# Kernel optimization log

Hardware: AMD Instinct MI355X
Metric: run time of the kernel (lower is better)

Reference implementation:

```python
import jax, jax.numpy as jnp
import numpy as np

B, L, D = 2, 1024, 768
NH, HD = 12, 64
NL = 6
MLP = 3072
THETA = 10000.0


def _rope(pos, dim, theta):
    # pos: (L,) float -> (L, dim//2, 2, 2) rotation matrices (FLUX rope)
    omega = 1.0 / (theta ** (jnp.arange(0, dim, 2, dtype=jnp.float32) / dim))
    out = pos[:, None] * omega  # (L, dim//2)
    cos, sin = jnp.cos(out), jnp.sin(out)
    return jnp.stack([jnp.stack([cos, -sin], -1), jnp.stack([sin, cos], -1)], -2)


def _build_pe(seq_len, pe_dim):
    # 2D spatial ids: axis0 = x (fast), axis1 = y (slow); axes_dim = [pe_dim//2, pe_dim//2]
    h = w = int(seq_len ** 0.5)
    y_ids = jnp.repeat(jnp.arange(h, dtype=jnp.float32), w)
    x_ids = jnp.tile(jnp.arange(w, dtype=jnp.float32), h)
    half = pe_dim // 2
    pe = jnp.concatenate([_rope(x_ids, half, THETA), _rope(y_ids, half, THETA)], axis=-3)
    return pe[None, None]  # (1, 1, L, pe_dim//2, 2, 2)


def _apply_rope(x, pe):
    # x: (B, H, L, HD)
    xs = x.reshape(x.shape[:-1] + (-1, 1, 2))
    out = pe[..., 0] * xs[..., 0] + pe[..., 1] * xs[..., 1]
    return out.reshape(x.shape)


def _rmsnorm(x, scale):
    return x * jax.lax.rsqrt(jnp.mean(x * x, axis=-1, keepdims=True) + 1e-6) * scale


def _layernorm(x, g, b):
    m = jnp.mean(x, axis=-1, keepdims=True)
    v = jnp.var(x, axis=-1, keepdims=True)
    return (x - m) * jax.lax.rsqrt(v + 1e-5) * g + b


def _forward(spatial_features, density_weights, condition_embeddings,
             spatial_w, spatial_b, cond_w, cond_b,
             ln1_g, ln1_b, qkv_w, q_scale, k_scale, proj_w, proj_b,
             dscale, dbias, ln2_g, ln2_b, mlp_w1, mlp_b1, mlp_w2, mlp_b2,
             out_w, out_b):
    Bsz, Ls, Ds = spatial_features.shape
    x = spatial_features @ spatial_w + spatial_b
    x = x + (condition_embeddings @ cond_w + cond_b)[:, None, :]
    pe = _build_pe(Ls, HD)
    dflat = density_weights.reshape(Bsz, 1, Ls)  # H*W == L, no interpolation
    attn_scale = HD ** -0.5
    for i in range(NL):
        h = _layernorm(x, ln1_g[i], ln1_b[i])
        qkv = (h @ qkv_w[i]).reshape(Bsz, Ls, 3, NH, HD).transpose(2, 0, 3, 1, 4)
        q, k, v = qkv[0], qkv[1], qkv[2]
        q = _rmsnorm(q, q_scale[i])
        k = _rmsnorm(k, k_scale[i])
        q = _apply_rope(q, pe)
        k = _apply_rope(k, pe)
        scores = jnp.einsum('bhld,bhmd->bhlm', q, k) * attn_scale
        scores = scores + (dscale[i] * dflat[..., None] + dbias[i])  # (B,1,L,1) bcast
        attn = jax.nn.softmax(scores, axis=-1)
        o = jnp.einsum('bhlm,bhmd->bhld', attn, v)
        o = o.transpose(0, 2, 1, 3).reshape(Bsz, Ls, Ds)
        x = x + o @ proj_w[i] + proj_b[i]
        h2 = _layernorm(x, ln2_g[i], ln2_b[i])
        x = x + jax.nn.gelu(h2 @ mlp_w1[i] + mlp_b1[i], approximate=False) @ mlp_w2[i] + mlp_b2[i]
    return x @ out_w + out_b


def setup_inputs() -> dict:
    key = jax.random.key(0)
    ks = jax.random.split(key, 16)
    s = 0.02
    inp = {
        'spatial_features': jax.random.normal(ks[0], (B, L, D), jnp.float32),
        'density_weights': jax.random.uniform(ks[1], (B, 32, 32), jnp.float32),
        'condition_embeddings': jax.random.normal(ks[2], (B, 1536), jnp.float32),
        'spatial_w': jax.random.normal(ks[3], (D, D), jnp.float32) * s,
        'spatial_b': jnp.zeros((D,), jnp.float32),
        'cond_w': jax.random.normal(ks[4], (1536, D), jnp.float32) * s,
        'cond_b': jnp.zeros((D,), jnp.float32),
        'ln1_g': jnp.ones((NL, D), jnp.float32),
        'ln1_b': jnp.zeros((NL, D), jnp.float32),
        'qkv_w': jax.random.normal(ks[5], (NL, D, 3 * D), jnp.float32) * s,
        'q_scale': jnp.ones((NL, HD), jnp.float32),
        'k_scale': jnp.ones((NL, HD), jnp.float32),
        'proj_w': jax.random.normal(ks[6], (NL, D, D), jnp.float32) * s,
        'proj_b': jnp.zeros((NL, D), jnp.float32),
        'dscale': jnp.ones((NL,), jnp.float32),
        'dbias': jnp.zeros((NL,), jnp.float32),
        'ln2_g': jnp.ones((NL, D), jnp.float32),
        'ln2_b': jnp.zeros((NL, D), jnp.float32),
        'mlp_w1': jax.random.normal(ks[7], (NL, D, MLP), jnp.float32) * s,
        'mlp_b1': jnp.zeros((NL, MLP), jnp.float32),
        'mlp_w2': jax.random.normal(ks[8], (NL, MLP, D), jnp.float32) * s,
        'mlp_b2': jnp.zeros((NL, D), jnp.float32),
        'out_w': jax.random.normal(ks[9], (D, D), jnp.float32) * s,
        'out_b': jnp.zeros((D,), jnp.float32),
    }
    return inp


def reference(spatial_features, density_weights, condition_embeddings,
              spatial_w, spatial_b, cond_w, cond_b,
              ln1_g, ln1_b, qkv_w, q_scale, k_scale, proj_w, proj_b,
              dscale, dbias, ln2_g, ln2_b, mlp_w1, mlp_b1, mlp_w2, mlp_b2,
              out_w, out_b):
    return _forward(spatial_features, density_weights, condition_embeddings,
                    spatial_w, spatial_b, cond_w, cond_b,
                    ln1_g, ln1_b, qkv_w, q_scale, k_scale, proj_w, proj_b,
                    dscale, dbias, ln2_g, ln2_b, mlp_w1, mlp_b1, mlp_w2, mlp_b2,
                    out_w, out_b)
```

## Files before the change

### kernel.cpp

```cpp
#include <hip/hip_runtime.h>
#include <hip/hip_bf16.h>
#include <cstdint>
#include <cstddef>

typedef unsigned short u16;
using short8  = __attribute__((ext_vector_type(8))) short;
using floatx4 = __attribute__((ext_vector_type(4))) float;

typedef __attribute__((address_space(1))) void gvoid;
typedef __attribute__((address_space(3))) void svoid;

__device__ __forceinline__ u16 f2bf(float f) {
  __hip_bfloat16 h = __float2bfloat16(f);
  return __builtin_bit_cast(u16, h);
}

__device__ __forceinline__ floatx4 mfma16(short8 a, short8 b, floatx4 c) {
  return __builtin_amdgcn_mfma_f32_16x16x32_bf16(a, b, c, 0, 0, 0);
}

__device__ __forceinline__ void glds16(const u16* g, u16* l) {
  __builtin_amdgcn_global_load_lds((gvoid*)g, (svoid*)l, 16, 0, 0);
}

__global__ void pe_kernel(float* __restrict__ pet) {
  int t = blockIdx.x * 256 + threadIdx.x;
  if (t >= 32768) return;
  int l = t >> 5, j = t & 31;
  float pos   = (j < 16) ? (float)(l & 31) : (float)(l >> 5);
  float omega = powf(10000.f, -(float)(j & 15) / 16.f);
  float a = pos * omega;
  pet[2 * t]     = cosf(a);
  pet[2 * t + 1] = sinf(a);
}

__global__ __launch_bounds__(256) void twt_kernel(const float* __restrict__ in,
                                                  u16* __restrict__ out, int K, int N) {
  size_t lofs = (size_t)blockIdx.z * K * N;
  in  += lofs;
  out += lofs;
  __shared__ float tile[32][33];
  int bx = blockIdx.x;
  int by = blockIdx.y;
  int tx = threadIdx.x & 31, ty = threadIdx.x >> 5;
  #pragma unroll
  for (int p = 0; p < 4; p++) {
    int k = by * 32 + ty + p * 8;
    tile[ty + p * 8][tx] = in[(size_t)k * N + bx * 32 + tx];
  }
  __syncthreads();
  #pragma unroll
  for (int p = 0; p < 4; p++) {
    int n = bx * 32 + ty + p * 8;
    out[(size_t)n * K + by * 32 + tx] = f2bf(tile[tx][ty + p * 8]);
  }
}

__global__ void cvt_kernel(const float* __restrict__ in, u16* __restrict__ out, int n) {
  int i = blockIdx.x * 256 + threadIdx.x;
  if (i < n) out[i] = f2bf(in[i]);
}

__global__ __launch_bounds__(256) void condp_kernel(const float* __restrict__ ce,
                                                    const float* __restrict__ w,
                                                    float* __restrict__ partial) {
  int d = blockIdx.x * 256 + threadIdx.x;
  int c = blockIdx.y;
  #pragma unroll
  for (int b = 0; b < 2; b++) {
    float acc = 0.f;
    #pragma unroll 4
    for (int k = c * 96; k < c * 96 + 96; k++) acc += ce[b * 1536 + k] * w[(size_t)k * 768 + d];
    partial[(size_t)(c * 2 + b) * 768 + d] = acc;
  }
}

__global__ __launch_bounds__(256) void condr_kernel(const float* __restrict__ partial,
                                                    const float* __restrict__ bias,
                                                    float* __restrict__ out) {
  int t = blockIdx.x * 256 + threadIdx.x;
  int b = t / 768, d = t % 768;
  float acc = bias[d];
  #pragma unroll
  for (int c = 0; c < 16; c++) acc += partial[(size_t)(c * 2 + b) * 768 + d];
  out[b * 768 + d] = acc;
}

__global__ __launch_bounds__(256) void ln_kernel(const float* __restrict__ x,
                                                 const float* __restrict__ g,
                                                 const float* __restrict__ b,
                                                 u16* __restrict__ out) {
  int row = blockIdx.x;
  const float* xr = x + (size_t)row * 768;
  int t = threadIdx.x;
  float v0 = xr[t], v1 = xr[t + 256], v2 = xr[t + 512];
  float s = v0 + v1 + v2, s2 = v0 * v0 + v1 * v1 + v2 * v2;
  #pragma unroll
  for (int o = 32; o >= 1; o >>= 1) { s += __shfl_xor(s, o); s2 += __shfl_xor(s2, o); }
  __shared__ float red[8];
  int w = t >> 6, lane = t & 63;
  if (lane == 0) { red[w] = s; red[4 + w] = s2; }
  __syncthreads();
  s  = red[0] + red[1] + red[2] + red[3];
  s2 = red[4] + red[5] + red[6] + red[7];
  float mean = s * (1.f / 768.f);
  float var  = s2 * (1.f / 768.f) - mean * mean;
  float rstd = rsqrtf(var + 1e-5f);
  u16* orow = out + (size_t)row * 768;
  orow[t]       = f2bf((v0 - mean) * rstd * g[t] + b[t]);
  orow[t + 256] = f2bf((v1 - mean) * rstd * g[t + 256] + b[t + 256]);
  orow[t + 512] = f2bf((v2 - mean) * rstd * g[t + 512] + b[t + 512]);
}

__global__ __launch_bounds__(256) void ropeq_kernel(const float* __restrict__ qkv,
                                                    const float* __restrict__ qs,
                                                    const float* __restrict__ ks,
                                                    const float* __restrict__ pet,
                                                    u16* __restrict__ qb, u16* __restrict__ kb) {
  int gid = blockIdx.x * 4 + (threadIdx.x >> 6);
  int lane = threadIdx.x & 63;
  int h = gid % 12, bl = gid / 12;
  int l = bl & 1023, b = bl >> 10;
  const float* qp = qkv + ((size_t)(b * 1024 + l) * 3 + 0) * 768 + h * 64;
  const float* kp = qp + 768;
  float q = qp[lane], k = kp[lane];
  float sq = q * q, sk = k * k;
  #pragma unroll
  for (int o = 1; o < 64; o <<= 1) { sq += __shfl_xor(sq, o); sk += __shfl_xor(sk, o); }
  q *= rsqrtf(sq * (1.f / 64.f) + 1e-6f) * qs[lane];
  k *= rsqrtf(sk * (1.f / 64.f) + 1e-6f) * ks[lane];
  int j = lane >> 1;
  float c = pet[(l * 32 + j) * 2], s = pet[(l * 32 + j) * 2 + 1];
  float qo = __shfl_xor(q, 1), ko = __shfl_xor(k, 1);
  float qr = (lane & 1) ? (s * qo + c * q) : (c * q - s * qo);
  float kr = (lane & 1) ? (s * ko + c * k) : (c * k - s * ko);
  int bh = b * 12 + h;
  qb[((size_t)bh * 1024 + l) * 64 + lane] = f2bf(qr * 0.125f);
  kb[((size_t)bh * 1024 + l) * 64 + lane] = f2bf(kr);
}

__global__ __launch_bounds__(256) void vtrans_kernel(const float* __restrict__ qkv,
                                                     u16* __restrict__ vt) {
  int lt = blockIdx.x, bh = blockIdx.y;
  int b = bh / 12, h = bh % 12;
  __shared__ float tile[64][65];
  int t = threadIdx.x, c = t & 63, r0 = t >> 6;
  #pragma unroll
  for (int p = 0; p < 16; p++) {
    int lr = p * 4 + r0;
    tile[lr][c] = qkv[((size_t)(b * 1024 + lt * 64 + lr) * 3 + 2) * 768 + h * 64 + c];
  }
  __syncthreads();
  #pragma unroll
  for (int p = 0; p < 16; p++) {
    int d = p * 4 + r0;
    vt[((size_t)bh * 64 + d) * 1024 + lt * 64 + c] = f2bf(tile[c][d]);
  }
}

__global__ __launch_bounds__(256) void attn_split(const u16* __restrict__ qb,
                                                  const u16* __restrict__ kbuf,
                                                  const u16* __restrict__ vt,
                                                  float* __restrict__ po,
                                                  float* __restrict__ pl) {
  const int qt = blockIdx.x, bh = blockIdx.y, sp = blockIdx.z;
  const int lane = threadIdx.x & 63, w = threadIdx.x >> 6;
  const int quad = lane >> 4, l16 = lane & 15;
  __shared__ __align__(16) u16 Ks[128 * 64];
  __shared__ __align__(16) u16 Vs[64 * 128];
  __shared__ __align__(16) u16 Ps[4][16 * 136];
  const u16* Q  = qb   + (size_t)bh * 1024 * 64;
  const u16* Kp = kbuf + (size_t)bh * 1024 * 64;
  const u16* Vp = vt   + (size_t)bh * 64 * 1024;
  const int qrow0 = qt * 64 + w * 16;
  short8 aq0, aq1;
  {
    const u16* qp = Q + (size_t)(qrow0 + l16) * 64 + quad * 8;
    aq0 = *(const short8*)qp;
    aq1 = *(const short8*)(qp + 32);
  }
  floatx4 accO[4];
  #pragma unroll
  for (int i = 0; i < 4; i++) accO[i] = (floatx4){0.f, 0.f, 0.f, 0.f};
  float lsum[4] = {0.f, 0.f, 0.f, 0.f};

  const int krow_in = (lane >> 3);
  const int kchunk  = lane & 7;
  const int vrow_in = (lane >> 4);
  const int vchunk  = lane & 15;

  for (int nt = 0; nt < 4; ++nt) {
    const int kb0 = sp * 512 + nt * 128;
    __syncthreads();
    #pragma unroll
    for (int j = 0; j < 4; j++) {
      int r = w * 32 + j * 8 + krow_in;
      int g = kchunk ^ (r & 7);
      glds16(Kp + (size_t)(kb0 + r) * 64 + g * 8, Ks + (w * 32 + j * 8) * 64);
    }
    #pragma unroll
    for (int j = 0; j < 4; j++) {
      int r = w * 16 + j * 4 + vrow_in;
      int g = vchunk ^ (r & 15);
      glds16(Vp + (size_t)r * 1024 + kb0 + g * 8, Vs + (w * 16 + j * 4) * 128);
    }
    __syncthreads();

    floatx4 s[8];
    #pragma unroll
    for (int n = 0; n < 8; n++) {
      int row = n * 16 + l16;
      int c0 = quad ^ (l16 & 7);
      short8 b0 = *(const short8*)&Ks[row * 64 + c0 * 8];
      short8 b1 = *(const short8*)&Ks[row * 64 + (c0 ^ 4) * 8];
      floatx4 z = (floatx4){0.f, 0.f, 0.f, 0.f};
      z = mfma16(aq0, b0, z);
      s[n] = mfma16(aq1, b1, z);
    }
    #pragma unroll
    for (int n = 0; n < 8; n++) {
      #pragma unroll
      for (int r = 0; r < 4; r++) {
        float pv = __expf(s[n][r] - 8.f);
        lsum[r] += pv;
        Ps[w][(quad * 4 + r) * 136 + n * 16 + l16] = f2bf(pv);
      }
    }
    #pragma unroll
    for (int kt = 0; kt < 4; kt++) {
      short8 ap = *(const short8*)&Ps[w][l16 * 136 + kt * 32 + quad * 8];
      #pragma unroll
      for (int dt = 0; dt < 4; dt++) {
        int vrow = dt * 16 + l16;
        int c = (kt * 4 + quad) ^ l16;
        short8 bv = *(const short8*)&Vs[vrow * 128 + c * 8];
        accO[dt] = mfma16(ap, bv, accO[dt]);
      }
    }
  }
  #pragma unroll
  for (int r = 0; r < 4; r++) {
    #pragma unroll
    for (int o = 1; o < 16; o <<= 1) lsum[r] += __shfl_xor(lsum[r], o);
  }
  const size_t sb = (size_t)(sp * 24 + bh) * 1024;
  #pragma unroll
  for (int r = 0; r < 4; r++) {
    int lr = qrow0 + quad * 4 + r;
    if (l16 == 0) pl[sb + lr] = lsum[r];
    #pragma unroll
    for (int dt = 0; dt < 4; dt++)
      po[(sb + lr) * 64 + dt * 16 + l16] = accO[dt][r];
  }
}

__global__ __launch_bounds__(256) void attn_comb(const float* __restrict__ po,
                                                 const float* __restrict__ pl,
                                                 u16* __restrict__ obuf) {
  int w = threadIdx.x >> 6, lane = threadIdx.x & 63;
  int gr = blockIdx.x * 4 + w;
  int bh = gr >> 10, l = gr & 1023;
  float num = 0.f, den = 0.f;
  #pragma unroll
  for (int s = 0; s < 2; s++) {
    num += po[((size_t)(s * 24 + bh) * 1024 + l) * 64 + lane];
    den += pl[(size_t)(s * 24 + bh) * 1024 + l];
  }
  int b = bh / 12, h = bh % 12;
  obuf[((size_t)(b * 1024 + l)) * 768 + h * 64 + lane] = f2bf(num / den);
}

template <int EPI, int BN>
__global__ __launch_bounds__(256) void gemm_bt(const u16* __restrict__ A,
                                               const u16* __restrict__ Bt,
                                               const float* __restrict__ bias,
                                               const float* extra,
                                               float* Cf, u16* Cb, int M, int N, int K) {
  constexpr int ROWS = 64 + BN;
  constexpr int RPW  = ROWS / 4;
  constexpr int NG   = RPW / 8;
  constexpr int NTW  = BN / 32;
  __shared__ __align__(16) u16 S[2][ROWS * 64];
  const int t = threadIdx.x;
  const int lane = t & 63, w = t >> 6;
  const int quad = lane >> 4, l16 = lane & 15;
  const int m0 = blockIdx.y * 64, n0 = blockIdx.x * BN;
  const int wm = (w >> 1) * 32, wn = (w & 1) * (BN / 2);

  floatx4 acc[2][NTW];
  #pragma unroll
  for (int i = 0; i < 2; i++)
    #pragma unroll
    for (int j = 0; j < NTW; j++) acc[i][j] = (floatx4){0.f, 0.f, 0.f, 0.f};

  const u16* gsrc[NG];
  int loff[NG];
  #pragma unroll
  for (int j = 0; j < NG; j++) {
    int r = w * RPW + j * 8 + (lane >> 3);
    int c = lane & 7;
    int g = c ^ (r & 7);
    const u16* base = (r < 64) ? (A + (size_t)(m0 + r) * K)
                               : (Bt + (size_t)(n0 + r - 64) * K);
    gsrc[j] = base + g * 8;
    loff[j] = (w * RPW + j * 8) * 64;
  }

  const int NIT = K >> 6;

  auto compute = [&](int buf) {
    #pragma unroll
    for (int kk = 0; kk < 2; kk++) {
      short8 af[2], bfr[NTW];
      #pragma unroll
      for (int mt = 0; mt < 2; mt++) {
        int ra = wm + mt * 16 + l16;
        af[mt] = *(const short8*)&S[buf][ra * 64 + ((((kk << 2) | quad)) ^ (ra & 7)) * 8];
      }
      #pragma unroll
      for (int nt = 0; nt < NTW; nt++) {
        int rb = 64 + wn + nt * 16 + l16;
        bfr[nt] = *(const short8*)&S[buf][rb * 64 + ((((kk << 2) | quad)) ^ (rb & 7)) * 8];
      }
      #pragma unroll
      for (int mt = 0; mt < 2; mt++)
        #pragma unroll
        for (int nt = 0; nt < NTW; nt++)
          acc[mt][nt] = mfma16(af[mt], bfr[nt], acc[mt][nt]);
    }
  };

  #pragma unroll
  for (int j = 0; j < NG; j++) glds16(gsrc[j], &S[0][loff[j]]);
  __syncthreads();

  int cur = 0;
  for (int it = 1; it < NIT; ++it) {
    #pragma unroll
    for (int j = 0; j < NG; j++) glds16(gsrc[j] + it * 64, &S[cur ^ 1][loff[j]]);
    compute(cur);
    __syncthreads();
    cur ^= 1;
  }
  compute(cur);

  #pragma unroll
  for (int mt = 0; mt < 2; mt++) {
    #pragma unroll
    for (int nt = 0; nt < NTW; nt++) {
      int col = n0 + wn + nt * 16 + l16;
      float bcol = bias ? bias[col] : 0.f;
      #pragma unroll
      for (int r = 0; r < 4; r++) {
        int row = m0 + wm + mt * 16 + quad * 4 + r;
        float v = acc[mt][nt][r] + bcol;
        if (EPI == 1) v += extra[(row >> 10) * N + col];
        if (EPI == 2) v += extra[(size_t)row * N + col];
        if (EPI == 3) v = 0.5f * v * (1.f + erff(v * 0.70710678118654752f));
        if (Cf) Cf[(size_t)row * N + col] = v;
        if (Cb) Cb[(size_t)row * N + col] = f2bf(v);
      }
    }
  }
}

extern "C" void kernel_launch(void* const* d_in, const int* in_sizes, int n_in,
                              void* d_out, int out_size, void* d_ws, size_t ws_size,
                              hipStream_t stream) {
  const float* sf   = (const float*)d_in[0];
  const float* ce   = (const float*)d_in[2];
  const float* sw   = (const float*)d_in[3];
  const float* sb   = (const float*)d_in[4];
  const float* cw   = (const float*)d_in[5];
  const float* cb   = (const float*)d_in[6];
  const float* ln1g = (const float*)d_in[7];
  const float* ln1b = (const float*)d_in[8];
  const float* qkvw = (const float*)d_in[9];
  const float* qsc  = (const float*)d_in[10];
  const float* ksc  = (const float*)d_in[11];
  const float* pw   = (const float*)d_in[12];
  const float* pb   = (const float*)d_in[13];
  const float* ln2g = (const float*)d_in[16];
  const float* ln2b = (const float*)d_in[17];
  const float* w1   = (const float*)d_in[18];
  const float* b1   = (const float*)d_in[19];
  const float* w2   = (const float*)d_in[20];
  const float* b2   = (const float*)d_in[21];
  const float* ow   = (const float*)d_in[22];
  const float* ob   = (const float*)d_in[23];

  char* p = (char*)d_ws;
  auto alloc = [&](size_t bytes) { char* r = p; p += (bytes + 255) & ~(size_t)255; return r; };
  float* pet  = (float*)alloc((size_t)1024 * 32 * 2 * 4);
  u16* swT    = (u16*)alloc((size_t)768 * 768 * 2);
  u16* owT    = (u16*)alloc((size_t)768 * 768 * 2);
  u16* qkvT   = (u16*)alloc((size_t)6 * 2304 * 768 * 2);
  u16* pwT    = (u16*)alloc((size_t)6 * 768 * 768 * 2);
  u16* w1T    = (u16*)alloc((size_t)6 * 3072 * 768 * 2);
  u16* w2T    = (u16*)alloc((size_t)6 * 768 * 3072 * 2);
  u16* sfb    = (u16*)alloc((size_t)2048 * 768 * 2);
  float* cpar = (float*)alloc((size_t)32 * 768 * 4);
  float* cond = (float*)alloc((size_t)2 * 768 * 4);
  float* x    = (float*)alloc((size_t)2048 * 768 * 4);
  u16* xb     = (u16*)alloc((size_t)2048 * 768 * 2);
  u16* h      = (u16*)alloc((size_t)2048 * 768 * 2);
  float* qkv  = (float*)alloc((size_t)2048 * 2304 * 4);
  u16* qbuf   = (u16*)alloc((size_t)2048 * 768 * 2);
  u16* kbuf   = (u16*)alloc((size_t)2048 * 768 * 2);
  u16* vtb    = (u16*)alloc((size_t)2048 * 768 * 2);
  u16* obuf   = (u16*)alloc((size_t)2048 * 768 * 2);
  u16* gbuf   = (u16*)alloc((size_t)2048 * 3072 * 2);
  float* po   = (float*)alloc((size_t)2 * 24 * 1024 * 64 * 4);
  float* pl   = (float*)alloc((size_t)2 * 24 * 1024 * 4);

  pe_kernel<<<128, 256, 0, stream>>>(pet);
  twt_kernel<<<dim3(24, 24, 1), 256, 0, stream>>>(sw, swT, 768, 768);
  twt_kernel<<<dim3(24, 24, 1), 256, 0, stream>>>(ow, owT, 768, 768);
  twt_kernel<<<dim3(72, 24, 6), 256, 0, stream>>>(qkvw, qkvT, 768, 2304);
  twt_kernel<<<dim3(24, 24, 6), 256, 0, stream>>>(pw, pwT, 768, 768);
  twt_kernel<<<dim3(96, 24, 6), 256, 0, stream>>>(w1, w1T, 768, 3072);
  twt_kernel<<<dim3(24, 96, 6), 256, 0, stream>>>(w2, w2T, 3072, 768);
  cvt_kernel<<<(2048 * 768) / 256, 256, 0, stream>>>(sf, sfb, 2048 * 768);
  condp_kernel<<<dim3(3, 16), 256, 0, stream>>>(ce, cw, cpar);
  condr_kernel<<<6, 256, 0, stream>>>(cpar, cb, cond);

  gemm_bt<1, 64><<<dim3(12, 32), 256, 0, stream>>>(sfb, swT, sb, cond, x, nullptr, 2048, 768, 768);

  for (int i = 0; i < 6; i++) {
    ln_kernel<<<2048, 256, 0, stream>>>(x, ln1g + i * 768, ln1b + i * 768, h);
    gemm_bt<0, 128><<<dim3(18, 32), 256, 0, stream>>>(h, qkvT + (size_t)i * 2304 * 768,
                                                      nullptr, nullptr, qkv, nullptr, 2048, 2304, 768);
    ropeq_kernel<<<6144, 256, 0, stream>>>(qkv, qsc + i * 64, ksc + i * 64, pet, qbuf, kbuf);
    vtrans_kernel<<<dim3(16, 24), 256, 0, stream>>>(qkv, vtb);
    attn_split<<<dim3(16, 24, 2), 256, 0, stream>>>(qbuf, kbuf, vtb, po, pl);
    attn_comb<<<6144, 256, 0, stream>>>(po, pl, obuf);
    gemm_bt<2, 64><<<dim3(12, 32), 256, 0, stream>>>(obuf, pwT + (size_t)i * 768 * 768,
                                                     pb + i * 768, x, x, xb, 2048, 768, 768);
    ln_kernel<<<2048, 256, 0, stream>>>(x, ln2g + i * 768, ln2b + i * 768, h);
    gemm_bt<3, 128><<<dim3(24, 32), 256, 0, stream>>>(h, w1T + (size_t)i * 3072 * 768,
                                                      b1 + i * 3072, nullptr, nullptr, gbuf, 2048, 3072, 768);
    gemm_bt<2, 64><<<dim3(12, 32), 256, 0, stream>>>(gbuf, w2T + (size_t)i * 768 * 3072,
                                                     b2 + i * 768, x, x, xb, 2048, 768, 3072);
  }
  gemm_bt<0, 64><<<dim3(12, 32), 256, 0, stream>>>(xb, owT, ob, nullptr, (float*)d_out, nullptr,
                                                   2048, 768, 768);
}
```

Measured before the change: 1.028 ms.

## Triple-buffer GEMM LDS tiles with partial vmcnt waits for deeper prefetch

Converts the bf16 GEMM main loop from double to triple buffering in LDS. Tiles are now prefetched two iterations ahead, and each iteration waits only on the older load group (s_waitcnt vmcnt(NG)) before a raw s_barrier. The aim is to hide more global-load latency behind MFMA compute. The cost is 50% more shared memory per block, which can lower occupancy, and a more fragile synchronisation scheme that relies on hand-written waitcnt.

```diff
diff --git a/kernel.cpp b/kernel.cpp
--- a/kernel.cpp
+++ b/kernel.cpp
@@ -280,7 +280,7 @@
   constexpr int RPW  = ROWS / 4;
   constexpr int NG   = RPW / 8;
   constexpr int NTW  = BN / 32;
-  __shared__ __align__(16) u16 S[2][ROWS * 64];
+  __shared__ __align__(16) u16 S[3][ROWS * 64];
   const int t = threadIdx.x;
   const int lane = t & 63, w = t >> 6;
   const int quad = lane >> 4, l16 = lane & 15;
@@ -309,18 +309,19 @@
   const int NIT = K >> 6;
 
   auto compute = [&](int buf) {
+    const u16* Sb = &S[buf][0];
     #pragma unroll
     for (int kk = 0; kk < 2; kk++) {
       short8 af[2], bfr[NTW];
       #pragma unroll
       for (int mt = 0; mt < 2; mt++) {
         int ra = wm + mt * 16 + l16;
-        af[mt] = *(const short8*)&S[buf][ra * 64 + ((((kk << 2) | quad)) ^ (ra & 7)) * 8];
+        af[mt] = *(const short8*)&Sb[ra * 64 + ((((kk << 2) | quad)) ^ (ra & 7)) * 8];
       }
       #pragma unroll
       for (int nt = 0; nt < NTW; nt++) {
         int rb = 64 + wn + nt * 16 + l16;
-        bfr[nt] = *(const short8*)&S[buf][rb * 64 + ((((kk << 2) | quad)) ^ (rb & 7)) * 8];
+        bfr[nt] = *(const short8*)&Sb[rb * 64 + ((((kk << 2) | quad)) ^ (rb & 7)) * 8];
       }
       #pragma unroll
       for (int mt = 0; mt < 2; mt++)
@@ -332,17 +333,28 @@
 
   #pragma unroll
   for (int j = 0; j < NG; j++) glds16(gsrc[j], &S[0][loff[j]]);
-  __syncthreads();
-
-  int cur = 0;
-  for (int it = 1; it < NIT; ++it) {
-    #pragma unroll
-    for (int j = 0; j < NG; j++) glds16(gsrc[j] + it * 64, &S[cur ^ 1][loff[j]]);
-    compute(cur);
-    __syncthreads();
-    cur ^= 1;
-  }
-  compute(cur);
+  #pragma unroll
+  for (int j = 0; j < NG; j++) glds16(gsrc[j] + 64, &S[1][loff[j]]);
+  asm volatile("s_waitcnt vmcnt(%0)" :: "n"(NG) : "memory");
+  __builtin_amdgcn_s_barrier();
+  asm volatile("" ::: "memory");
+
+  int bufc = 0;
+  for (int it = 0; it < NIT; ++it) {
+    if (it + 2 < NIT) {
+      int bufp = bufc + 2; if (bufp >= 3) bufp -= 3;
+      #pragma unroll
+      for (int j = 0; j < NG; j++) glds16(gsrc[j] + (it + 2) * 64, &S[bufp][loff[j]]);
+    }
+    compute(bufc);
+    if (it + 1 < NIT) {
+      if (it + 2 < NIT) asm volatile("s_waitcnt vmcnt(%0)" :: "n"(NG) : "memory");
+      else              asm volatile("s_waitcnt vmcnt(0)" ::: "memory");
+      __builtin_amdgcn_s_barrier();
+      asm volatile("" ::: "memory");
+    }
+    bufc = (bufc + 1 == 3) ? 0 : bufc + 1;
+  }
 
   #pragma unroll
   for (int mt = 0; mt < 2; mt++) {
```

New measurement: 1.018 ms. No clear change (-1.0%).
